# Kernel optimization log

Measured on AMD Instinct MI355X. Metric: run time of the kernel, lower is better.

Reference implementation:

```python
import jax, jax.numpy as jnp
import numpy as np

N_NODES = 100_000
N_EDGES = 1_600_000
DIM_IN = 256
ADD_TO_EDGE_SCORE = 0.5  # PyG EdgePooling default


def setup_inputs() -> dict:
    key = jax.random.key(0)
    k1, k2, k3 = jax.random.split(key, 3)
    x = jax.random.normal(k1, (N_NODES, DIM_IN), dtype=jnp.float32)
    edge_index = jax.random.randint(k2, (2, N_EDGES), 0, N_NODES, dtype=jnp.int32)
    batch = jnp.zeros((N_NODES,), dtype=jnp.int32)  # single graph
    W = jax.random.normal(k3, (2 * DIM_IN, 1), dtype=jnp.float32) / np.sqrt(2.0 * DIM_IN)
    b = jnp.zeros((1,), dtype=jnp.float32)
    return {"x": x, "edge_index": edge_index, "batch": batch, "W": W, "b": b}


def _segment_softmax(scores, seg, num_segments):
    m = jax.ops.segment_max(scores, seg, num_segments=num_segments)
    ex = jnp.exp(scores - m[seg])
    s = jax.ops.segment_sum(ex, seg, num_segments=num_segments)
    return ex / s[seg]


def _greedy_matching(rank, src, dst, num_nodes):
    """Maximal matching equivalent to sequential greedy over edges sorted by
    ascending rank (rank = position in descending-score argsort, a strict total
    order). Implemented as parallel locally-dominant matching rounds."""
    big = jnp.iinfo(jnp.int32).max

    def cond(state):
        alive, matched, chosen = state
        return jnp.any(alive)

    def body(state):
        alive, matched, chosen = state
        r = jnp.where(alive, rank, big)
        node_min = jnp.full((num_nodes,), big, dtype=jnp.int32)
        node_min = node_min.at[src].min(r)
        node_min = node_min.at[dst].min(r)
        # an alive edge is picked if it dominates all alive edges at both endpoints
        pick = alive & (rank == node_min[src]) & (rank == node_min[dst])
        matched = matched.at[jnp.where(pick, src, num_nodes)].set(True, mode='drop')
        matched = matched.at[jnp.where(pick, dst, num_nodes)].set(True, mode='drop')
        chosen = chosen | pick
        alive = alive & ~matched[src] & ~matched[dst]
        return alive, matched, chosen

    alive0 = jnp.ones_like(rank, dtype=bool)
    matched0 = jnp.zeros((num_nodes,), dtype=bool)
    chosen0 = jnp.zeros_like(alive0)
    _, matched, chosen = jax.lax.while_loop(cond, body, (alive0, matched0, chosen0))
    return chosen, matched


def reference(x, edge_index, batch, W, b):
    num_nodes, feat = x.shape
    num_edges = edge_index.shape[1]
    src, dst = edge_index[0], edge_index[1]

    # Linear([x_src || x_dst]) split to avoid materializing [E, 2F]
    s_src = x @ W[:feat, 0]   # [N]
    s_dst = x @ W[feat:, 0]   # [N]
    raw = s_src[src] + s_dst[dst] + b[0]            # [E]
    # dropout is identity in eval mode
    e = _segment_softmax(raw, dst, num_nodes) + ADD_TO_EDGE_SCORE  # [E]

    # rank: position of each edge in descending-score order
    order = jnp.argsort(-e)
    rank = jnp.zeros((num_edges,), dtype=jnp.int32).at[order].set(
        jnp.arange(num_edges, dtype=jnp.int32))

    chosen, matched = _greedy_matching(rank, src, dst, num_nodes)

    # cluster id of each chosen edge = its position among chosen edges in score order
    chosen_sorted = chosen[order]
    cid_sorted = jnp.cumsum(chosen_sorted.astype(jnp.int32)) - 1
    cid = jnp.zeros((num_edges,), dtype=jnp.int32).at[order].set(cid_sorted)
    num_matched = jnp.sum(chosen.astype(jnp.int32))

    # node -> cluster assignment; unmatched nodes get trailing singleton clusters
    cluster = jnp.zeros((num_nodes,), dtype=jnp.int32)
    cluster = cluster.at[jnp.where(chosen, src, num_nodes)].set(cid, mode='drop')
    cluster = cluster.at[jnp.where(chosen, dst, num_nodes)].set(cid, mode='drop')
    unm = num_matched + jnp.cumsum((~matched).astype(jnp.int32)) - 1
    cluster = jnp.where(matched, cluster, unm)
    num_clusters = num_matched + jnp.sum((~matched).astype(jnp.int32))

    # per-cluster score: chosen-edge scores for merged pairs, 1.0 for singletons
    new_edge_score = jnp.ones((num_nodes,), dtype=x.dtype)
    new_edge_score = new_edge_score.at[jnp.where(chosen, cid, num_nodes)].set(e, mode='drop')

    # scatter-merge node features (rows >= num_clusters are zero padding)
    new_x = jax.ops.segment_sum(x, cluster, num_segments=num_nodes)
    new_x = new_x * new_edge_score[:, None]

    new_edge_index = cluster[edge_index]  # remapped edges (coalesce/dedup omitted)
    new_batch = jnp.zeros((num_nodes,), dtype=batch.dtype).at[cluster].set(batch)

    return new_x, new_edge_index, new_batch, num_clusters
```

## Files before the change

kernel.cpp:

```cpp
#include <hip/hip_runtime.h>

typedef unsigned int u32;
typedef unsigned long long u64;
typedef unsigned char u8;

static constexpr int SORTN = 65536;
static constexpr int STILE = 2048;
static constexpr int NR    = 28;
static constexpr int NHEAVY= 3;
static constexpr int NXCD  = 8;

__device__ __forceinline__ u32 xccid() {
  u32 x;
  asm volatile("s_getreg_b32 %0, hwreg(HW_REG_XCC_ID)" : "=s"(x));
  return x & (NXCD - 1);
}

__device__ __forceinline__ void wmin64(u64* p, u64 v) {
  __hip_atomic_fetch_min(p, v, __ATOMIC_RELAXED, __HIP_MEMORY_SCOPE_WORKGROUP);
}
__device__ __forceinline__ void wmax32(u32* p, u32 v) {
  __hip_atomic_fetch_max(p, v, __ATOMIC_RELAXED, __HIP_MEMORY_SCOPE_WORKGROUP);
}
__device__ __forceinline__ void waddf64(double* p, double v) {
  __hip_atomic_fetch_add(p, v, __ATOMIC_RELAXED, __HIP_MEMORY_SCOPE_WORKGROUP);
}

__device__ __forceinline__ u32 ordf(float f) {
  u32 u = __float_as_uint(f);
  return (u & 0x80000000u) ? ~u : (u | 0x80000000u);
}
__device__ __forceinline__ float inv_ordf(u32 m) {
  return __uint_as_float((m & 0x80000000u) ? (m ^ 0x80000000u) : ~m);
}

__global__ __launch_bounds__(256)
void k_init(u32* m_ord, u32* m8, double* ssum, double* ss8, u8* matched,
            u64* node_min, u64* nm8, float* scoreC, ulonglong2* sortbuf,
            u32* fcnt, u32* scalars, int N, int E) {
  int i = blockIdx.x * blockDim.x + threadIdx.x;
  if (i < N) { m_ord[i] = 0u; ssum[i] = 0.0; matched[i] = 0; scoreC[i] = 1.0f; }
  if (i < 2 * N) node_min[i] = ~0ull;
  if (i < NXCD * N) { nm8[i] = ~0ull; m8[i] = 0u; ss8[i] = 0.0; }
  if (i < SORTN) sortbuf[i] = make_ulonglong2(~0ull, ~0ull);
  if (i < 256)   fcnt[i] = 0u;
  if (i < 16)    scalars[i] = 0u;
  if (i == 0)    fcnt[0] = (u32)E;
}

__global__ __launch_bounds__(256)
void k_dots(const float4* __restrict__ x4, const float4* __restrict__ W4,
            float* __restrict__ s_src, float* __restrict__ s_dst, int N) {
  int gt = blockIdx.x * blockDim.x + threadIdx.x;
  int w = gt >> 6, lane = gt & 63;
  if (w >= N) return;
  float4 xa = x4[(size_t)w * 64 + lane];
  float4 wa = W4[lane];
  float4 wb = W4[64 + lane];
  float pa = xa.x*wa.x + xa.y*wa.y + xa.z*wa.z + xa.w*wa.w;
  float pb = xa.x*wb.x + xa.y*wb.y + xa.z*wb.z + xa.w*wb.w;
  #pragma unroll
  for (int m = 32; m >= 1; m >>= 1) {
    pa += __shfl_xor(pa, m);
    pb += __shfl_xor(pb, m);
  }
  if (lane == 0) { s_src[w] = pa; s_dst[w] = pb; }
}

__global__ __launch_bounds__(256)
void k_max8(const int* __restrict__ src, const int* __restrict__ dst,
            const float* __restrict__ s_src, const float* __restrict__ s_dst,
            const float* __restrict__ bvec, u32* m8, float* __restrict__ raw,
            int N, int E) {
  int e = blockIdx.x * blockDim.x + threadIdx.x;
  if (e >= E) return;
  u32* mW = m8 + (size_t)xccid() * N;
  int d = dst[e];
  float r = s_src[src[e]] + s_dst[d] + bvec[0];
  raw[e] = r;
  wmax32(&mW[d], ordf(r));
}

__global__ __launch_bounds__(256)
void k_maxmerge(const u32* __restrict__ m8, u32* __restrict__ m_ord, int N) {
  int v = blockIdx.x * 256 + threadIdx.x;
  if (v >= N) return;
  u32 m = 0u;
  #pragma unroll
  for (int x = 0; x < NXCD; x++) {
    u32 t = m8[(size_t)x * N + v];
    m = (t > m) ? t : m;
  }
  m_ord[v] = m;
}

__global__ __launch_bounds__(256)
void k_expsum8(const int* __restrict__ dst, const float* __restrict__ raw,
               const u32* __restrict__ m_ord, double* ss8, int N, int E) {
  int e = blockIdx.x * blockDim.x + threadIdx.x;
  if (e >= E) return;
  double* sW = ss8 + (size_t)xccid() * N;
  int d = dst[e];
  float ex = expf(raw[e] - inv_ordf(m_ord[d]));
  waddf64(&sW[d], (double)ex);
}

__global__ __launch_bounds__(256)
void k_ssmerge(const double* __restrict__ ss8, double* __restrict__ ssum, int N) {
  int v = blockIdx.x * 256 + threadIdx.x;
  if (v >= N) return;
  double s = 0.0;
  #pragma unroll
  for (int x = 0; x < NXCD; x++) s += ss8[(size_t)x * N + v];
  ssum[v] = s;
}

__global__ __launch_bounds__(256)
void k_scorekey(const int* __restrict__ src, const int* __restrict__ dst,
                const float* __restrict__ raw, const u32* __restrict__ m_ord,
                const double* __restrict__ ssum,
                ulonglong2* __restrict__ front0, u64* nm8, int N, int E) {
  int e = blockIdx.x * blockDim.x + threadIdx.x;
  if (e >= E) return;
  u64* nmW = nm8 + (size_t)xccid() * N;
  int s = src[e], d = dst[e];
  float ex = expf(raw[e] - inv_ordf(m_ord[d]));
  float es = ex / (float)ssum[d] + 0.5f;
  u64 key = ((u64)(~ordf(es)) << 32) | (u32)e;
  u64 sd  = ((u64)(u32)s << 32) | (u32)d;
  front0[e] = make_ulonglong2(key, sd);
  wmin64(&nmW[s], key);
  if (d != s) wmin64(&nmW[d], key);
}

__global__ __launch_bounds__(256)
void k_merge(u64* nm8, u64* __restrict__ nmOut, int N) {
  int v = blockIdx.x * 256 + threadIdx.x;
  if (v >= N) return;
  u64 m = ~0ull;
  #pragma unroll
  for (int x = 0; x < NXCD; x++) {
    size_t idx = (size_t)x * N + v;
    u64 t = nm8[idx];
    if (t != ~0ull) { nm8[idx] = ~0ull; m = (t < m) ? t : m; }
  }
  nmOut[v] = m;
}

template<int R>
__global__ __launch_bounds__(256)
void k_mmin_h(const ulonglong2* __restrict__ fin, const u32* __restrict__ cntp,
              const u8* __restrict__ matched, u64* nm8, int N) {
  u32 cnt = *cntp;
  u64* nmW = nm8 + (size_t)xccid() * N;
  u32 nth = gridDim.x * 256;
  for (u32 i = blockIdx.x * 256 + threadIdx.x; i < cnt; i += nth) {
    ulonglong2 t = fin[i];
    int s = (int)(t.y >> 32), d = (int)(u32)t.y;
    if (matched[s] | matched[d]) continue;
    wmin64(&nmW[s], t.x);
    if (d != s) wmin64(&nmW[d], t.x);
  }
}

template<int R>
__global__ __launch_bounds__(256)
void k_mmin_l(const ulonglong2* __restrict__ fin, const u32* __restrict__ cntp,
              const u8* __restrict__ matched, u64* nm) {
  u32 cnt = *cntp;
  u32 nth = gridDim.x * 256;
  for (u32 i = blockIdx.x * 256 + threadIdx.x; i < cnt; i += nth) {
    ulonglong2 t = fin[i];
    int s = (int)(t.y >> 32), d = (int)(u32)t.y;
    if (matched[s] | matched[d]) continue;
    atomicMin(&nm[s], t.x);
    if (d != s) atomicMin(&nm[d], t.x);
  }
}

template<int R>
__global__ __launch_bounds__(256)
void k_mpick(const ulonglong2* __restrict__ fin, const u32* __restrict__ cntp,
             const u64* __restrict__ nm, u64* nmNext, u8* matched,
             ulonglong2* fout, u32* cntOut, ulonglong2* sortbuf, u32* scalars) {
  __shared__ u32 wb[4];
  __shared__ u32 bbase;
  u32 cnt = *cntp;
  int tx = threadIdx.x, lane = tx & 63, wid = tx >> 6;
  for (u32 base = blockIdx.x * 256; base < cnt; base += gridDim.x * 256) {
    u32 gid = base + tx;
    ulonglong2 t = make_ulonglong2(0ull, 0ull);
    int s = 0, d = 0;
    bool pk = false, surv = false;
    if (gid < cnt) {
      t = fin[gid];
      s = (int)(t.y >> 32); d = (int)(u32)t.y;
      if (!(matched[s] | matched[d])) {
        pk = (nm[s] == t.x) && (nm[d] == t.x);
        surv = !pk;
      }
    }
    u64 pm = __ballot(pk);
    if (pm) {
      u32 pre = (u32)__popcll(pm & ((1ull << lane) - 1ull));
      int ldr = __ffsll((long long)pm) - 1;
      u32 pb = 0;
      if (lane == ldr) pb = atomicAdd(&scalars[0], (u32)__popcll(pm));
      pb = __shfl(pb, ldr);
      if (pk) { matched[s] = 1; matched[d] = 1; sortbuf[pb + pre] = t; }
    }
    u64 sm = __ballot(surv);
    if (lane == 0) wb[wid] = (u32)__popcll(sm);
    __syncthreads();
    if (tx == 0) {
      u32 tt = wb[0] + wb[1] + wb[2] + wb[3];
      bbase = tt ? atomicAdd(cntOut, tt) : 0u;
    }
    __syncthreads();
    if (surv) {
      u32 woff = 0;
      for (int w = 0; w < wid; w++) woff += wb[w];
      u32 pre = (u32)__popcll(sm & ((1ull << lane) - 1ull));
      fout[bbase + woff + pre] = t;
      nmNext[s] = ~0ull;
      if (d != s) nmNext[d] = ~0ull;
    }
    __syncthreads();
  }
}

__global__ __launch_bounds__(1024)
void k_mfinish(ulonglong2* fA, ulonglong2* fB, u8* matched, u64* nmA, u64* nmB,
               ulonglong2* sortbuf, const u32* __restrict__ cntp, u32* scalars) {
  __shared__ u32 sh_cnt;
  u32 cnt = *cntp;
  int tx = threadIdx.x;
  ulonglong2* fin = fA; ulonglong2* fout = fB;
  u64* nmCur = nmA; u64* nmNxt = nmB;
  while (cnt > 0) {
    if (tx == 0) sh_cnt = 0;
    __syncthreads();
    for (u32 i = tx; i < cnt; i += 1024) {
      ulonglong2 t = fin[i];
      int s = (int)(t.y >> 32), d = (int)(u32)t.y;
      if (matched[s] | matched[d]) continue;
      wmin64(&nmCur[s], t.x);
      if (d != s) wmin64(&nmCur[d], t.x);
    }
    __syncthreads();
    for (u32 i = tx; i < cnt; i += 1024) {
      ulonglong2 t = fin[i];
      int s = (int)(t.y >> 32), d = (int)(u32)t.y;
      if (matched[s] | matched[d]) continue;
      u64 a = __hip_atomic_fetch_add(&nmCur[s], 0ull, __ATOMIC_RELAXED,
                                     __HIP_MEMORY_SCOPE_WORKGROUP);
      u64 b = (d == s) ? a
            : __hip_atomic_fetch_add(&nmCur[d], 0ull, __ATOMIC_RELAXED,
                                     __HIP_MEMORY_SCOPE_WORKGROUP);
      if (a == t.x && b == t.x) {
        matched[s] = 1; matched[d] = 1;
        u32 o = atomicAdd(&scalars[0], 1u);
        sortbuf[o] = t;
      } else {
        u32 o = atomicAdd(&sh_cnt, 1u);
        fout[o] = t;
        nmNxt[s] = ~0ull;
        if (d != s) nmNxt[d] = ~0ull;
      }
    }
    __syncthreads();
    cnt = sh_cnt;
    ulonglong2* tf = fin; fin = fout; fout = tf;
    u64* tn = nmCur; nmCur = nmNxt; nmNxt = tn;
    __syncthreads();
  }
}

__global__ __launch_bounds__(256)
void k_sort1(ulonglong2* buf) {
  __shared__ ulonglong2 t[STILE];
  const int base = blockIdx.x * STILE;
  for (int i = threadIdx.x; i < STILE; i += 256) t[i] = buf[base + i];
  __syncthreads();
  for (int k = 2; k <= STILE; k <<= 1) {
    for (int j = k >> 1; j > 0; j >>= 1) {
      for (int i = threadIdx.x; i < STILE; i += 256) {
        int p = i ^ j;
        if (p > i) {
          bool dir = (((base + i) & k) == 0);
          ulonglong2 a = t[i], c = t[p];
          if ((a.x > c.x) == dir) { t[i] = c; t[p] = a; }
        }
      }
      __syncthreads();
    }
  }
  for (int i = threadIdx.x; i < STILE; i += 256) buf[base + i] = t[i];
}

__global__ __launch_bounds__(256)
void k_gpass(ulonglong2* buf, int j, int k) {
  int i = blockIdx.x * 256 + threadIdx.x;
  int p = i ^ j;
  if (p > i && p < SORTN) {
    bool dir = ((i & k) == 0);
    ulonglong2 a = buf[i], c = buf[p];
    if ((a.x > c.x) == dir) { buf[i] = c; buf[p] = a; }
  }
}

__global__ __launch_bounds__(256)
void k_sortl(ulonglong2* buf, int k) {
  __shared__ ulonglong2 t[STILE];
  const int base = blockIdx.x * STILE;
  const bool dir = ((base & k) == 0);
  for (int i = threadIdx.x; i < STILE; i += 256) t[i] = buf[base + i];
  __syncthreads();
  for (int j = STILE >> 1; j > 0; j >>= 1) {
    for (int i = threadIdx.x; i < STILE; i += 256) {
      int p = i ^ j;
      if (p > i) {
        ulonglong2 a = t[i], c = t[p];
        if ((a.x > c.x) == dir) { t[i] = c; t[p] = a; }
      }
    }
    __syncthreads();
  }
  for (int i = threadIdx.x; i < STILE; i += 256) buf[base + i] = t[i];
}

__global__ __launch_bounds__(256)
void k_assign(const ulonglong2* __restrict__ buf,
              int* cluster, int* memA, int* memB, float* scoreC,
              const u32* __restrict__ scalars) {
  int i = blockIdx.x * blockDim.x + threadIdx.x;
  if (i >= (int)scalars[0]) return;
  ulonglong2 t = buf[i];
  int s = (int)(t.y >> 32), d = (int)(u32)t.y;
  cluster[s] = i; cluster[d] = i;
  scoreC[i] = inv_ordf(~(u32)(t.x >> 32));
  memA[i] = s;
  memB[i] = (s == d) ? -1 : d;
}

__global__ __launch_bounds__(256)
void k_scan1(const u8* __restrict__ matched, u32* partials, int N) {
  __shared__ u32 sh[256];
  int b = blockIdx.x, tx = threadIdx.x;
  int v0 = b * 1024 + tx * 4;
  u32 c = 0;
  #pragma unroll
  for (int q = 0; q < 4; q++) { int v = v0 + q; if (v < N && !matched[v]) c++; }
  sh[tx] = c; __syncthreads();
  for (int s = 128; s > 0; s >>= 1) { if (tx < s) sh[tx] += sh[tx + s]; __syncthreads(); }
  if (tx == 0) partials[b] = sh[0];
}

__global__ void k_scan2(const u32* partials, u32* partials2, u32* scalars, int NB) {
  if (blockIdx.x == 0 && threadIdx.x == 0) {
    u32 run = 0;
    for (int i = 0; i < NB; i++) { partials2[i] = run; run += partials[i]; }
    scalars[1] = run;
    scalars[2] = scalars[0] + run;
  }
}

__global__ __launch_bounds__(256)
void k_scan3(const u8* __restrict__ matched, const u32* __restrict__ partials2,
             const u32* __restrict__ scalars, int* cluster, int* memA, int* memB, int N) {
  __shared__ u32 sh[256];
  int b = blockIdx.x, tx = threadIdx.x;
  int v0 = b * 1024 + tx * 4;
  u32 f[4]; u32 c = 0;
  #pragma unroll
  for (int q = 0; q < 4; q++) { int v = v0 + q; f[q] = (v < N && !matched[v]); c += f[q]; }
  sh[tx] = c; __syncthreads();
  for (int s = 1; s < 256; s <<= 1) {
    u32 x = sh[tx];
    u32 y = (tx >= s) ? sh[tx - s] : 0;
    __syncthreads();
    sh[tx] = x + y;
    __syncthreads();
  }
  u32 base = scalars[0] + partials2[b] + (sh[tx] - c);
  #pragma unroll
  for (int q = 0; q < 4; q++) {
    if (f[q]) {
      int v = v0 + q;
      int cc = (int)base++;
      cluster[v] = cc; memA[cc] = v; memB[cc] = -1;
    }
  }
}

__global__ __launch_bounds__(256)
void k_newx(const float4* __restrict__ x4, const int* __restrict__ memA,
            const int* __restrict__ memB, const float* __restrict__ scoreC,
            const u32* __restrict__ scalars, float4* __restrict__ out4, int N) {
  int gt = blockIdx.x * blockDim.x + threadIdx.x;
  int w = gt >> 6, lane = gt & 63;
  if (w >= N) return;
  int nc = (int)scalars[2];
  float4 o;
  if (w < nc) {
    int a = memA[w], b = memB[w];
    float s = scoreC[w];
    float4 va = x4[(size_t)a * 64 + lane];
    float ox = va.x, oy = va.y, oz = va.z, ow = va.w;
    if (b >= 0) {
      float4 vb = x4[(size_t)b * 64 + lane];
      ox += vb.x; oy += vb.y; oz += vb.z; ow += vb.w;
    }
    o = make_float4(ox * s, oy * s, oz * s, ow * s);
  } else {
    o = make_float4(0.f, 0.f, 0.f, 0.f);
  }
  out4[(size_t)w * 64 + lane] = o;
}

__global__ __launch_bounds__(256)
void k_remap(const int* __restrict__ ei, const int* __restrict__ cluster,
             float* __restrict__ outE, float* __restrict__ outB,
             const u32* __restrict__ scalars, int twoE, int N) {
  int i = blockIdx.x * blockDim.x + threadIdx.x;
  if (i < twoE) outE[i] = (float)cluster[ei[i]];
  int j = i - twoE;
  if (j >= 0 && j < N) outB[j] = 0.0f;
  if (j == N) outB[N] = (float)scalars[2];
}

template<int R>
static void launch_rounds(ulonglong2* frontA, ulonglong2* frontB, u64* nm8,
                          u64* node_min, u8* matched, ulonglong2* sortbuf,
                          u32* fcnt, u32* scalars, int N, int NB_E,
                          hipStream_t stream) {
  if constexpr (R < NR) {
    ulonglong2* fin  = (R & 1) ? frontB : frontA;
    ulonglong2* fout = (R & 1) ? frontA : frontB;
    u64* nm  = node_min + (size_t)(R & 1) * N;
    u64* nmN = node_min + (size_t)((R & 1) ^ 1) * N;
    int nbr = (R < 30) ? (NB_E >> R) : 0; if (nbr < 64) nbr = 64;
    if constexpr (R == 0) {
    } else if constexpr (R < NHEAVY) {
      k_mmin_h<R><<<nbr, 256, 0, stream>>>(fin, fcnt + R, matched, nm8, N);
      k_merge<<<(N + 255) / 256, 256, 0, stream>>>(nm8, nm, N);
    } else {
      k_mmin_l<R><<<nbr, 256, 0, stream>>>(fin, fcnt + R, matched, nm);
    }
    k_mpick<R><<<nbr, 256, 0, stream>>>(fin, fcnt + R, nm, nmN, matched,
                                        fout, fcnt + R + 1, sortbuf, scalars);
    launch_rounds<R + 1>(frontA, frontB, nm8, node_min, matched, sortbuf,
                         fcnt, scalars, N, NB_E, stream);
  }
}

extern "C" void kernel_launch(void* const* d_in, const int* in_sizes, int n_in,
                              void* d_out, int out_size, void* d_ws, size_t ws_size,
                              hipStream_t stream) {
  const float* x    = (const float*)d_in[0];
  const int*   ei   = (const int*)d_in[1];
  const float* W    = (const float*)d_in[3];
  const float* bvec = (const float*)d_in[4];
  int N = in_sizes[2];
  int E = in_sizes[1] / 2;

  char* p = (char*)d_ws;
  auto alloc = [&](size_t bytes) { char* r = p; p += (bytes + 255) & ~(size_t)255; return r; };
  float*      s_src    = (float*)alloc((size_t)N * 4);
  float*      s_dst    = (float*)alloc((size_t)N * 4);
  u32*        m_ord    = (u32*)alloc((size_t)N * 4);
  u32*        m8       = (u32*)alloc((size_t)NXCD * N * 4);
  double*     ssum     = (double*)alloc((size_t)N * 8);
  double*     ss8      = (double*)alloc((size_t)NXCD * N * 8);
  float*      raw      = (float*)alloc((size_t)E * 4);
  ulonglong2* frontA   = (ulonglong2*)alloc((size_t)E * 16);
  ulonglong2* frontB   = (ulonglong2*)alloc((size_t)E * 16);
  u8*         matched  = (u8*)alloc((size_t)N);
  u64*        node_min = (u64*)alloc((size_t)2 * N * 8);
  u64*        nm8      = (u64*)alloc((size_t)NXCD * N * 8);
  ulonglong2* sortbuf  = (ulonglong2*)alloc((size_t)SORTN * 16);
  int*        cluster  = (int*)alloc((size_t)N * 4);
  int*        memA     = (int*)alloc((size_t)N * 4);
  int*        memB     = (int*)alloc((size_t)N * 4);
  float*      scoreC   = (float*)alloc((size_t)N * 4);
  u32*        fcnt     = (u32*)alloc(1024);
  u32*        partials = (u32*)alloc(4096);
  u32*        partials2= (u32*)alloc(4096);
  u32*        scalars  = (u32*)alloc(256);
  (void)ws_size; (void)out_size; (void)n_in;

  const int* srcp = ei;
  const int* dstp = ei + E;
  float* out  = (float*)d_out;
  float* outX = out;
  float* outE = out + (size_t)N * 256;
  float* outB = outE + (size_t)2 * E;

  int NB_E = (E + 255) / 256;
  int cover = NXCD * N; if (cover < SORTN) cover = SORTN;
  k_init<<<(cover + 255) / 256, 256, 0, stream>>>(m_ord, m8, ssum, ss8, matched,
                                                  node_min, nm8, scoreC, sortbuf,
                                                  fcnt, scalars, N, E);
  k_dots<<<((size_t)N * 64 + 255) / 256, 256, 0, stream>>>(
      (const float4*)x, (const float4*)W, s_src, s_dst, N);
  k_max8<<<NB_E, 256, 0, stream>>>(srcp, dstp, s_src, s_dst, bvec, m8, raw, N, E);
  k_maxmerge<<<(N + 255) / 256, 256, 0, stream>>>(m8, m_ord, N);
  k_expsum8<<<NB_E, 256, 0, stream>>>(dstp, raw, m_ord, ss8, N, E);
  k_ssmerge<<<(N + 255) / 256, 256, 0, stream>>>(ss8, ssum, N);
  k_scorekey<<<NB_E, 256, 0, stream>>>(srcp, dstp, raw, m_ord, ssum,
                                       frontA, nm8, N, E);
  k_merge<<<(N + 255) / 256, 256, 0, stream>>>(nm8, node_min, N);

  launch_rounds<0>(frontA, frontB, nm8, node_min, matched, sortbuf, fcnt, scalars,
                   N, NB_E, stream);
  k_mfinish<<<1, 1024, 0, stream>>>(frontA, frontB, matched,
                                    node_min, node_min + N,
                                    sortbuf, fcnt + NR, scalars);

  k_sort1<<<SORTN / STILE, 256, 0, stream>>>(sortbuf);
  for (int k = STILE << 1; k <= SORTN; k <<= 1) {
    for (int j = k >> 1; j >= STILE; j >>= 1)
      k_gpass<<<SORTN / 256, 256, 0, stream>>>(sortbuf, j, k);
    k_sortl<<<SORTN / STILE, 256, 0, stream>>>(sortbuf, k);
  }

  k_assign<<<SORTN / 256, 256, 0, stream>>>(sortbuf, cluster, memA, memB, scoreC, scalars);
  int NB = (N + 1023) / 1024;
  k_scan1<<<NB, 256, 0, stream>>>(matched, partials, N);
  k_scan2<<<1, 64, 0, stream>>>(partials, partials2, scalars, NB);
  k_scan3<<<NB, 256, 0, stream>>>(matched, partials2, scalars, cluster, memA, memB, N);

  k_newx<<<((size_t)N * 64 + 255) / 256, 256, 0, stream>>>(
      (const float4*)x, memA, memB, scoreC, scalars, (float4*)outX, N);
  k_remap<<<(2 * E + N + 1 + 255) / 256, 256, 0, stream>>>(
      ei, cluster, outE, outB, scalars, 2 * E, N);
}
```

Baseline: 1.470 ms.

## Split edge frontier into key/endpoint arrays, add nontemporal accesses, retune rounds and sort tile

Replaces the 16-byte interleaved frontier records with separate key and src/dst arrays, so the min-reduction passes read the endpoints first and load the key only for live edges. k_max8 now writes the packed endpoints once, and k_scorekey reads them instead of re-reading src and dst. Streaming loads and stores are marked nontemporal to keep them from polluting cache. The number of launched matching rounds drops from 28 to 20, handing more of the tail to the single-block finisher, and the sort tile grows to 4096. The risk is a longer serial finish loop and worse locality from the split arrays.

```diff
diff --git a/kernel.cpp b/kernel.cpp
--- a/kernel.cpp
+++ b/kernel.cpp
@@ -5,8 +5,8 @@
 typedef unsigned char u8;
 
 static constexpr int SORTN = 65536;
-static constexpr int STILE = 2048;
-static constexpr int NR    = 28;
+static constexpr int STILE = 4096;
+static constexpr int NR    = 20;
 static constexpr int NHEAVY= 3;
 static constexpr int NXCD  = 8;
 
@@ -24,6 +24,20 @@
 }
 __device__ __forceinline__ void waddf64(double* p, double v) {
   __hip_atomic_fetch_add(p, v, __ATOMIC_RELAXED, __HIP_MEMORY_SCOPE_WORKGROUP);
+}
+
+typedef __attribute__((ext_vector_type(4))) float evf4;
+template <typename T>
+__device__ __forceinline__ T ntl(const T* p) { return __builtin_nontemporal_load(p); }
+template <typename T>
+__device__ __forceinline__ void nts(T v, T* p) { __builtin_nontemporal_store(v, p); }
+__device__ __forceinline__ float4 ntl4(const float4* p) {
+  evf4 v = __builtin_nontemporal_load((const evf4*)p);
+  return make_float4(v.x, v.y, v.z, v.w);
+}
+__device__ __forceinline__ void nts4(float4 v, float4* p) {
+  evf4 t; t.x = v.x; t.y = v.y; t.z = v.z; t.w = v.w;
+  __builtin_nontemporal_store(t, (evf4*)p);
 }
 
 __device__ __forceinline__ u32 ordf(float f) {
@@ -54,7 +68,7 @@
   int gt = blockIdx.x * blockDim.x + threadIdx.x;
   int w = gt >> 6, lane = gt & 63;
   if (w >= N) return;
-  float4 xa = x4[(size_t)w * 64 + lane];
+  float4 xa = ntl4(&x4[(size_t)w * 64 + lane]);
   float4 wa = W4[lane];
   float4 wb = W4[64 + lane];
   float pa = xa.x*wa.x + xa.y*wa.y + xa.z*wa.z + xa.w*wa.w;
@@ -71,13 +85,14 @@
 void k_max8(const int* __restrict__ src, const int* __restrict__ dst,
             const float* __restrict__ s_src, const float* __restrict__ s_dst,
             const float* __restrict__ bvec, u32* m8, float* __restrict__ raw,
-            int N, int E) {
+            u64* __restrict__ frontS, int N, int E) {
   int e = blockIdx.x * blockDim.x + threadIdx.x;
   if (e >= E) return;
   u32* mW = m8 + (size_t)xccid() * N;
-  int d = dst[e];
-  float r = s_src[src[e]] + s_dst[d] + bvec[0];
-  raw[e] = r;
+  int s = ntl(&src[e]), d = ntl(&dst[e]);
+  float r = s_src[s] + s_dst[d] + bvec[0];
+  nts(r, &raw[e]);
+  nts(((u64)(u32)s << 32) | (u32)d, &frontS[e]);
   wmax32(&mW[d], ordf(r));
 }
 
@@ -100,8 +115,8 @@
   int e = blockIdx.x * blockDim.x + threadIdx.x;
   if (e >= E) return;
   double* sW = ss8 + (size_t)xccid() * N;
-  int d = dst[e];
-  float ex = expf(raw[e] - inv_ordf(m_ord[d]));
+  int d = ntl(&dst[e]);
+  float ex = expf(ntl(&raw[e]) - inv_ordf(m_ord[d]));
   waddf64(&sW[d], (double)ex);
 }
 
@@ -116,19 +131,18 @@
 }
 
 __global__ __launch_bounds__(256)
-void k_scorekey(const int* __restrict__ src, const int* __restrict__ dst,
-                const float* __restrict__ raw, const u32* __restrict__ m_ord,
-                const double* __restrict__ ssum,
-                ulonglong2* __restrict__ front0, u64* nm8, int N, int E) {
+void k_scorekey(const u64* __restrict__ frontS, const float* __restrict__ raw,
+                const u32* __restrict__ m_ord, const double* __restrict__ ssum,
+                u64* __restrict__ frontK, u64* nm8, int N, int E) {
   int e = blockIdx.x * blockDim.x + threadIdx.x;
   if (e >= E) return;
   u64* nmW = nm8 + (size_t)xccid() * N;
-  int s = src[e], d = dst[e];
-  float ex = expf(raw[e] - inv_ordf(m_ord[d]));
+  u64 sd = ntl(&frontS[e]);
+  int s = (int)(sd >> 32), d = (int)(u32)sd;
+  float ex = expf(ntl(&raw[e]) - inv_ordf(m_ord[d]));
   float es = ex / (float)ssum[d] + 0.5f;
   u64 key = ((u64)(~ordf(es)) << 32) | (u32)e;
-  u64 sd  = ((u64)(u32)s << 32) | (u32)d;
-  front0[e] = make_ulonglong2(key, sd);
+  nts(key, &frontK[e]);
   wmin64(&nmW[s], key);
   if (d != s) wmin64(&nmW[d], key);
 }
@@ -149,54 +163,59 @@
 
 template<int R>
 __global__ __launch_bounds__(256)
-void k_mmin_h(const ulonglong2* __restrict__ fin, const u32* __restrict__ cntp,
-              const u8* __restrict__ matched, u64* nm8, int N) {
+void k_mmin_h(const u64* __restrict__ fK, const u64* __restrict__ fS,
+              const u32* __restrict__ cntp, const u8* __restrict__ matched,
+              u64* nm8, int N) {
   u32 cnt = *cntp;
   u64* nmW = nm8 + (size_t)xccid() * N;
   u32 nth = gridDim.x * 256;
   for (u32 i = blockIdx.x * 256 + threadIdx.x; i < cnt; i += nth) {
-    ulonglong2 t = fin[i];
-    int s = (int)(t.y >> 32), d = (int)(u32)t.y;
+    u64 sd = ntl(&fS[i]);
+    int s = (int)(sd >> 32), d = (int)(u32)sd;
     if (matched[s] | matched[d]) continue;
-    wmin64(&nmW[s], t.x);
-    if (d != s) wmin64(&nmW[d], t.x);
+    u64 k = ntl(&fK[i]);
+    wmin64(&nmW[s], k);
+    if (d != s) wmin64(&nmW[d], k);
   }
 }
 
 template<int R>
 __global__ __launch_bounds__(256)
-void k_mmin_l(const ulonglong2* __restrict__ fin, const u32* __restrict__ cntp,
-              const u8* __restrict__ matched, u64* nm) {
+void k_mmin_l(const u64* __restrict__ fK, const u64* __restrict__ fS,
+              const u32* __restrict__ cntp, const u8* __restrict__ matched,
+              u64* nm) {
   u32 cnt = *cntp;
   u32 nth = gridDim.x * 256;
   for (u32 i = blockIdx.x * 256 + threadIdx.x; i < cnt; i += nth) {
-    ulonglong2 t = fin[i];
-    int s = (int)(t.y >> 32), d = (int)(u32)t.y;
+    u64 sd = ntl(&fS[i]);
+    int s = (int)(sd >> 32), d = (int)(u32)sd;
     if (matched[s] | matched[d]) continue;
-    atomicMin(&nm[s], t.x);
-    if (d != s) atomicMin(&nm[d], t.x);
+    u64 k = ntl(&fK[i]);
+    atomicMin(&nm[s], k);
+    if (d != s) atomicMin(&nm[d], k);
   }
 }
 
 template<int R>
 __global__ __launch_bounds__(256)
-void k_mpick(const ulonglong2* __restrict__ fin, const u32* __restrict__ cntp,
-             const u64* __restrict__ nm, u64* nmNext, u8* matched,
-             ulonglong2* fout, u32* cntOut, ulonglong2* sortbuf, u32* scalars) {
+void k_mpick(const u64* __restrict__ fKin, const u64* __restrict__ fSin,
+             const u32* __restrict__ cntp, const u64* __restrict__ nm,
+             u64* nmNext, u8* matched, u64* fKout, u64* fSout, u32* cntOut,
+             ulonglong2* sortbuf, u32* scalars) {
   __shared__ u32 wb[4];
   __shared__ u32 bbase;
   u32 cnt = *cntp;
   int tx = threadIdx.x, lane = tx & 63, wid = tx >> 6;
   for (u32 base = blockIdx.x * 256; base < cnt; base += gridDim.x * 256) {
     u32 gid = base + tx;
-    ulonglong2 t = make_ulonglong2(0ull, 0ull);
+    u64 k = 0, sd = 0;
     int s = 0, d = 0;
     bool pk = false, surv = false;
     if (gid < cnt) {
-      t = fin[gid];
-      s = (int)(t.y >> 32); d = (int)(u32)t.y;
+      k = ntl(&fKin[gid]); sd = ntl(&fSin[gid]);
+      s = (int)(sd >> 32); d = (int)(u32)sd;
       if (!(matched[s] | matched[d])) {
-        pk = (nm[s] == t.x) && (nm[d] == t.x);
+        pk = (nm[s] == k) && (nm[d] == k);
         surv = !pk;
       }
     }
@@ -207,7 +226,7 @@
       u32 pb = 0;
       if (lane == ldr) pb = atomicAdd(&scalars[0], (u32)__popcll(pm));
       pb = __shfl(pb, ldr);
-      if (pk) { matched[s] = 1; matched[d] = 1; sortbuf[pb + pre] = t; }
+      if (pk) { matched[s] = 1; matched[d] = 1; sortbuf[pb + pre] = make_ulonglong2(k, sd); }
     }
     u64 sm = __ballot(surv);
     if (lane == 0) wb[wid] = (u32)__popcll(sm);
@@ -221,7 +240,9 @@
       u32 woff = 0;
       for (int w = 0; w < wid; w++) woff += wb[w];
       u32 pre = (u32)__popcll(sm & ((1ull << lane) - 1ull));
-      fout[bbase + woff + pre] = t;
+      u32 o = bbase + woff + pre;
+      nts(k, &fKout[o]);
+      nts(sd, &fSout[o]);
       nmNext[s] = ~0ull;
       if (d != s) nmNext[d] = ~0ull;
     }
@@ -230,48 +251,53 @@
 }
 
 __global__ __launch_bounds__(1024)
-void k_mfinish(ulonglong2* fA, ulonglong2* fB, u8* matched, u64* nmA, u64* nmB,
-               ulonglong2* sortbuf, const u32* __restrict__ cntp, u32* scalars) {
+void k_mfinish(u64* fKA, u64* fSA, u64* fKB, u64* fSB, u8* matched,
+               u64* nmA, u64* nmB, ulonglong2* sortbuf,
+               const u32* __restrict__ cntp, u32* scalars) {
   __shared__ u32 sh_cnt;
   u32 cnt = *cntp;
   int tx = threadIdx.x;
-  ulonglong2* fin = fA; ulonglong2* fout = fB;
-  u64* nmCur = nmA; u64* nmNxt = nmB;
+  u64 *fKin = fKA, *fSin = fSA, *fKout = fKB, *fSout = fSB;
+  u64 *nmCur = nmA, *nmNxt = nmB;
   while (cnt > 0) {
     if (tx == 0) sh_cnt = 0;
     __syncthreads();
     for (u32 i = tx; i < cnt; i += 1024) {
-      ulonglong2 t = fin[i];
-      int s = (int)(t.y >> 32), d = (int)(u32)t.y;
+      u64 sd = fSin[i];
+      int s = (int)(sd >> 32), d = (int)(u32)sd;
       if (matched[s] | matched[d]) continue;
-      wmin64(&nmCur[s], t.x);
-      if (d != s) wmin64(&nmCur[d], t.x);
+      u64 k = fKin[i];
+      wmin64(&nmCur[s], k);
+      if (d != s) wmin64(&nmCur[d], k);
     }
     __syncthreads();
     for (u32 i = tx; i < cnt; i += 1024) {
-      ulonglong2 t = fin[i];
-      int s = (int)(t.y >> 32), d = (int)(u32)t.y;
+      u64 sd = fSin[i];
+      int s = (int)(sd >> 32), d = (int)(u32)sd;
       if (matched[s] | matched[d]) continue;
+      u64 k = fKin[i];
       u64 a = __hip_atomic_fetch_add(&nmCur[s], 0ull, __ATOMIC_RELAXED,
                                      __HIP_MEMORY_SCOPE_WORKGROUP);
       u64 b = (d == s) ? a
             : __hip_atomic_fetch_add(&nmCur[d], 0ull, __ATOMIC_RELAXED,
                                      __HIP_MEMORY_SCOPE_WORKGROUP);
-      if (a == t.x && b == t.x) {
+      if (a == k && b == k) {
         matched[s] = 1; matched[d] = 1;
         u32 o = atomicAdd(&scalars[0], 1u);
-        sortbuf[o] = t;
+        sortbuf[o] = make_ulonglong2(k, sd);
       } else {
         u32 o = atomicAdd(&sh_cnt, 1u);
-        fout[o] = t;
+        fKout[o] = k; fSout[o] = sd;
         nmNxt[s] = ~0ull;
         if (d != s) nmNxt[d] = ~0ull;
       }
     }
     __syncthreads();
     cnt = sh_cnt;
-    ulonglong2* tf = fin; fin = fout; fout = tf;
-    u64* tn = nmCur; nmCur = nmNxt; nmNxt = tn;
+    u64* t;
+    t = fKin; fKin = fKout; fKout = t;
+    t = fSin; fSin = fSout; fSout = t;
+    t = nmCur; nmCur = nmNxt; nmNxt = t;
     __syncthreads();
   }
 }
@@ -405,17 +431,17 @@
   if (w < nc) {
     int a = memA[w], b = memB[w];
     float s = scoreC[w];
-    float4 va = x4[(size_t)a * 64 + lane];
+    float4 va = ntl4(&x4[(size_t)a * 64 + lane]);
     float ox = va.x, oy = va.y, oz = va.z, ow = va.w;
     if (b >= 0) {
-      float4 vb = x4[(size_t)b * 64 + lane];
+      float4 vb = ntl4(&x4[(size_t)b * 64 + lane]);
       ox += vb.x; oy += vb.y; oz += vb.z; ow += vb.w;
     }
     o = make_float4(ox * s, oy * s, oz * s, ow * s);
   } else {
     o = make_float4(0.f, 0.f, 0.f, 0.f);
   }
-  out4[(size_t)w * 64 + lane] = o;
+  nts4(o, &out4[(size_t)w * 64 + lane]);
 }
 
 __global__ __launch_bounds__(256)
@@ -423,33 +449,35 @@
              float* __restrict__ outE, float* __restrict__ outB,
              const u32* __restrict__ scalars, int twoE, int N) {
   int i = blockIdx.x * blockDim.x + threadIdx.x;
-  if (i < twoE) outE[i] = (float)cluster[ei[i]];
+  if (i < twoE) nts((float)cluster[ntl(&ei[i])], &outE[i]);
   int j = i - twoE;
   if (j >= 0 && j < N) outB[j] = 0.0f;
   if (j == N) outB[N] = (float)scalars[2];
 }
 
 template<int R>
-static void launch_rounds(ulonglong2* frontA, ulonglong2* frontB, u64* nm8,
+static void launch_rounds(u64* fKA, u64* fSA, u64* fKB, u64* fSB, u64* nm8,
                           u64* node_min, u8* matched, ulonglong2* sortbuf,
                           u32* fcnt, u32* scalars, int N, int NB_E,
                           hipStream_t stream) {
   if constexpr (R < NR) {
-    ulonglong2* fin  = (R & 1) ? frontB : frontA;
-    ulonglong2* fout = (R & 1) ? frontA : frontB;
+    u64* fKin  = (R & 1) ? fKB : fKA;
+    u64* fSin  = (R & 1) ? fSB : fSA;
+    u64* fKout = (R & 1) ? fKA : fKB;
+    u64* fSout = (R & 1) ? fSA : fSB;
     u64* nm  = node_min + (size_t)(R & 1) * N;
     u64* nmN = node_min + (size_t)((R & 1) ^ 1) * N;
     int nbr = (R < 30) ? (NB_E >> R) : 0; if (nbr < 64) nbr = 64;
     if constexpr (R == 0) {
     } else if constexpr (R < NHEAVY) {
-      k_mmin_h<R><<<nbr, 256, 0, stream>>>(fin, fcnt + R, matched, nm8, N);
+      k_mmin_h<R><<<nbr, 256, 0, stream>>>(fKin, fSin, fcnt + R, matched, nm8, N);
       k_merge<<<(N + 255) / 256, 256, 0, stream>>>(nm8, nm, N);
     } else {
-      k_mmin_l<R><<<nbr, 256, 0, stream>>>(fin, fcnt + R, matched, nm);
-    }
-    k_mpick<R><<<nbr, 256, 0, stream>>>(fin, fcnt + R, nm, nmN, matched,
-                                        fout, fcnt + R + 1, sortbuf, scalars);
-    launch_rounds<R + 1>(frontA, frontB, nm8, node_min, matched, sortbuf,
+      k_mmin_l<R><<<nbr, 256, 0, stream>>>(fKin, fSin, fcnt + R, matched, nm);
+    }
+    k_mpick<R><<<nbr, 256, 0, stream>>>(fKin, fSin, fcnt + R, nm, nmN, matched,
+                                        fKout, fSout, fcnt + R + 1, sortbuf, scalars);
+    launch_rounds<R + 1>(fKA, fSA, fKB, fSB, nm8, node_min, matched, sortbuf,
                          fcnt, scalars, N, NB_E, stream);
   }
 }
@@ -473,8 +501,10 @@
   double*     ssum     = (double*)alloc((size_t)N * 8);
   double*     ss8      = (double*)alloc((size_t)NXCD * N * 8);
   float*      raw      = (float*)alloc((size_t)E * 4);
-  ulonglong2* frontA   = (ulonglong2*)alloc((size_t)E * 16);
-  ulonglong2* frontB   = (ulonglong2*)alloc((size_t)E * 16);
+  u64*        fKA      = (u64*)alloc((size_t)E * 8);
+  u64*        fSA      = (u64*)alloc((size_t)E * 8);
+  u64*        fKB      = (u64*)alloc((size_t)E * 8);
+  u64*        fSB      = (u64*)alloc((size_t)E * 8);
   u8*         matched  = (u8*)alloc((size_t)N);
   u64*        node_min = (u64*)alloc((size_t)2 * N * 8);
   u64*        nm8      = (u64*)alloc((size_t)NXCD * N * 8);
@@ -503,17 +533,16 @@
                                                   fcnt, scalars, N, E);
   k_dots<<<((size_t)N * 64 + 255) / 256, 256, 0, stream>>>(
       (const float4*)x, (const float4*)W, s_src, s_dst, N);
-  k_max8<<<NB_E, 256, 0, stream>>>(srcp, dstp, s_src, s_dst, bvec, m8, raw, N, E);
+  k_max8<<<NB_E, 256, 0, stream>>>(srcp, dstp, s_src, s_dst, bvec, m8, raw, fSA, N, E);
   k_maxmerge<<<(N + 255) / 256, 256, 0, stream>>>(m8, m_ord, N);
   k_expsum8<<<NB_E, 256, 0, stream>>>(dstp, raw, m_ord, ss8, N, E);
   k_ssmerge<<<(N + 255) / 256, 256, 0, stream>>>(ss8, ssum, N);
-  k_scorekey<<<NB_E, 256, 0, stream>>>(srcp, dstp, raw, m_ord, ssum,
-                                       frontA, nm8, N, E);
+  k_scorekey<<<NB_E, 256, 0, stream>>>(fSA, raw, m_ord, ssum, fKA, nm8, N, E);
   k_merge<<<(N + 255) / 256, 256, 0, stream>>>(nm8, node_min, N);
 
-  launch_rounds<0>(frontA, frontB, nm8, node_min, matched, sortbuf, fcnt, scalars,
-                   N, NB_E, stream);
-  k_mfinish<<<1, 1024, 0, stream>>>(frontA, frontB, matched,
+  launch_rounds<0>(fKA, fSA, fKB, fSB, nm8, node_min, matched, sortbuf,
+                   fcnt, scalars, N, NB_E, stream);
+  k_mfinish<<<1, 1024, 0, stream>>>(fKA, fSA, fKB, fSB, matched,
                                     node_min, node_min + N,
                                     sortbuf, fcnt + NR, scalars);
 
```

Result: slower. 1.613 ms (+9.7%).
